# Optimization experiments

Hardware: AMD Instinct MI355X
Metric: run time of the kernel (lower is better)

Reference implementation:

```python
import jax, jax.numpy as jnp
import numpy as np

T, B, H, V, L = 512, 8, 256, 32000, 3
THRESH = 1.0

# Heaviside spike with ATan surrogate gradient (snntorch default, alpha=2)
@jax.custom_vjp
def spike(u):
    return (u > 0).astype(u.dtype)

def _spike_fwd(u):
    return (u > 0).astype(u.dtype), u

def _spike_bwd(u, g):
    return (g / (1.0 + (jnp.pi * u) ** 2),)

spike.defvjp(_spike_fwd, _spike_bwd)


def leaky_scan(cur, beta):
    """mem[t] = beta * mem[t-1] + cur[t]; cur: (T,B,H), beta: (H,). No reset -> associative."""
    def step(mem, c):
        mem = beta * mem + c
        return mem, mem
    _, mems = jax.lax.scan(step, jnp.zeros(cur.shape[1:], cur.dtype), cur)
    return mems  # (T,B,H)


def setup_inputs() -> dict:
    key = jax.random.key(0)
    ks = jax.random.split(key, 10)
    s = 1.0 / np.sqrt(H)
    return {
        "tokens": jax.random.randint(ks[0], (T, B), 0, V),
        "token_emb": jax.random.normal(ks[1], (V, H), dtype=jnp.float32) * 0.02,
        "pos_emb": jax.random.normal(ks[2], (T, H), dtype=jnp.float32) * 0.02,
        "Wq": jax.random.normal(ks[3], (L, H, H), dtype=jnp.float32) * s,
        "bq": jnp.zeros((L, H), dtype=jnp.float32),
        "beta": jax.random.uniform(ks[4], (L, H), minval=0.5, maxval=0.95),
        "Wfc": jax.random.normal(ks[5], (L, H, H), dtype=jnp.float32) * s,
        "bfc": jnp.zeros((L, H), dtype=jnp.float32),
        "Wout": jax.random.normal(ks[6], (H, V), dtype=jnp.float32) * s,
        "bout": jnp.zeros((V,), dtype=jnp.float32),
    }


def reference(tokens, token_emb, pos_emb, Wq, bq, beta, Wfc, bfc, Wout, bout):
    # embed: (T,B,H) + broadcast positional (T,1,H)
    h = token_emb[tokens] + pos_emb[:, None, :]
    for l in range(L):  # small fixed layer count
        cur = jnp.einsum('tbh,hd->tbd', h, Wq[l]) + bq[l]   # q-projection
        mem = leaky_scan(cur, beta[l])                       # leaky integrate, no reset
        spk = spike(mem - THRESH)                            # heaviside spikes
        h = jax.nn.relu(jnp.einsum('tbh,hd->tbd', spk, Wfc[l]) + bfc[l])
    logits = jnp.einsum('tbh,hv->tbv', h, Wout) + bout       # (T,B,V)
    return logits
```

## Files before the change

kernel.cpp:

```cpp
#include <hip/hip_runtime.h>
#include <hip/hip_bf16.h>
#include <cstddef>

constexpr int T_ = 512;
constexpr int B_ = 8;
constexpr int H_ = 256;
constexpr int V_ = 32000;
constexpr int L_ = 3;
constexpr int M_ = T_ * B_;

typedef __attribute__((ext_vector_type(8))) short short8;
typedef __attribute__((ext_vector_type(4))) float floatx4;

__device__ __forceinline__ unsigned short f2bf(float f) {
    unsigned u = __float_as_uint(f);
    u += 0x7fffu + ((u >> 16) & 1u);
    return (unsigned short)(u >> 16);
}

__device__ __forceinline__ void gl_lds16(const void* g, void* l) {
    __builtin_amdgcn_global_load_lds((__attribute__((address_space(1))) void*)g,
                                     (__attribute__((address_space(3))) void*)l,
                                     16, 0, 0);
}

__global__ __launch_bounds__(256) void embed_kernel(
    const int* __restrict__ tokens, const float* __restrict__ temb,
    const float* __restrict__ pemb, unsigned short* __restrict__ hb)
{
    const int idx = blockIdx.x * 256 + threadIdx.x;
    const int h4 = idx & (H_ / 4 - 1);
    const int tb = idx >> 6;
    const int b  = tb & (B_ - 1);
    const int t  = tb >> 3;
    const int tok = tokens[t * B_ + b];
    const float4 e = *(const float4*)&temb[(size_t)tok * H_ + h4 * 4];
    const float4 p = *(const float4*)&pemb[(size_t)t * H_ + h4 * 4];
    ushort4 r;
    r.x = f2bf(e.x + p.x); r.y = f2bf(e.y + p.y);
    r.z = f2bf(e.z + p.z); r.w = f2bf(e.w + p.w);
    *(ushort4*)&hb[(size_t)idx * 4] = r;
}

__global__ __launch_bounds__(256) void scan_spike_lds(
    const float* __restrict__ cur, const float* __restrict__ beta_l,
    unsigned short* __restrict__ spk)
{
    __shared__ float buf[2][32][256];
    const int b = blockIdx.x;
    const int tid = threadIdx.x;
    const float bt = beta_l[tid];
    const float* base = cur + (size_t)b * H_;
    unsigned short* qb = spk + (size_t)b * H_ + tid;
    constexpr int CH = 32;
    constexpr int NC = T_ / CH;
    constexpr size_t TS = (size_t)B_ * H_;

    float4 regs[8];
    #pragma unroll
    for (int i = 0; i < 8; ++i) {
        const int fi = tid + 256 * i, r = fi >> 6, x = fi & 63;
        regs[i] = *(const float4*)&base[(size_t)r * TS + x * 4];
    }
    #pragma unroll
    for (int i = 0; i < 8; ++i) {
        const int fi = tid + 256 * i, r = fi >> 6, x = fi & 63;
        *(float4*)&buf[0][r][x * 4] = regs[i];
    }

    float mem = 0.0f;
    for (int c = 0; c < NC; ++c) {
        __syncthreads();
        if (c + 1 < NC) {
            #pragma unroll
            for (int i = 0; i < 8; ++i) {
                const int fi = tid + 256 * i, r = fi >> 6, x = fi & 63;
                regs[i] = *(const float4*)&base[(size_t)((c + 1) * CH + r) * TS + x * 4];
            }
        }
        const int p = c & 1;
        #pragma unroll
        for (int tt = 0; tt < CH; ++tt) {
            mem = fmaf(bt, mem, buf[p][tt][tid]);
            qb[(size_t)(c * CH + tt) * TS] = (mem > 1.0f) ? (unsigned short)0x3F80u
                                                          : (unsigned short)0u;
        }
        if (c + 1 < NC) {
            #pragma unroll
            for (int i = 0; i < 8; ++i) {
                const int fi = tid + 256 * i, r = fi >> 6, x = fi & 63;
                *(float4*)&buf[(c + 1) & 1][r][x * 4] = regs[i];
            }
        }
    }
}

__global__ __launch_bounds__(256) void transpose_small_kernel(
    const float* __restrict__ Wq, const float* __restrict__ Wfc,
    unsigned short* __restrict__ WT)
{
    __shared__ float t[64][65];
    const int z = blockIdx.z;
    const float* src = (z < 3) ? Wq + (size_t)z * H_ * H_
                               : Wfc + (size_t)(z - 3) * H_ * H_;
    unsigned short* dst = WT + (size_t)z * H_ * H_;
    const int n0 = blockIdx.x * 64, k0 = blockIdx.y * 64;
    const int x = threadIdx.x & 63, y = threadIdx.x >> 6;
    #pragma unroll
    for (int i = 0; i < 16; ++i)
        t[y + 4 * i][x] = src[(size_t)(k0 + y + 4 * i) * H_ + n0 + x];
    __syncthreads();
    #pragma unroll
    for (int i = 0; i < 16; ++i)
        dst[(size_t)(n0 + y + 4 * i) * H_ + k0 + x] = f2bf(t[x][y + 4 * i]);
}

__global__ __launch_bounds__(256) void transpose_wout_kernel(
    const float* __restrict__ W, unsigned short* __restrict__ Wt)
{
    __shared__ float t[64][65];
    const int n0 = blockIdx.x * 64;
    const int k0 = blockIdx.y * 64;
    const int x = threadIdx.x & 63, y = threadIdx.x >> 6;
    #pragma unroll
    for (int i = 0; i < 16; ++i)
        t[y + 4 * i][x] = W[(size_t)(k0 + y + 4 * i) * V_ + n0 + x];
    __syncthreads();
    #pragma unroll
    for (int i = 0; i < 16; ++i)
        Wt[(size_t)(n0 + y + 4 * i) * H_ + k0 + x] = f2bf(t[x][y + 4 * i]);
}


__global__ __launch_bounds__(256) void gemm_mfma_out(
    const unsigned short* __restrict__ A,
    const unsigned short* __restrict__ Bt,
    const float* __restrict__ bias,
    float* __restrict__ C)
{
    constexpr int K = H_, N = V_;
    __shared__ __align__(16) short lA[1024][8];
    __shared__ __align__(16) short lB[1024][8];

    const int tid = threadIdx.x;
    const int lane = tid & 63, wave = tid >> 6;
    const int wm = wave >> 1, wn = wave & 1;
    const int l15 = lane & 15, quad = lane >> 4;
    const int m0 = blockIdx.x * 128;
    const int n0 = blockIdx.y * 128;

    floatx4 acc[4][4] = {};

    for (int k0 = 0; k0 < K; k0 += 64) {
        #pragma unroll
        for (int j = 0; j < 4; ++j) {
            const int base = (wave * 4 + j) * 64;
            const int s = base + lane;
            const int row = s >> 3;
            const int oct = (s & 7) ^ (row & 7);
            gl_lds16(A  + (size_t)(m0 + row) * K + k0 + oct * 8, &lA[base][0]);
            gl_lds16(Bt + (size_t)(n0 + row) * K + k0 + oct * 8, &lB[base][0]);
        }
        __syncthreads();

        #pragma unroll
        for (int t = 0; t < 2; ++t) {
            short8 af[4], bf[4];
            #pragma unroll
            for (int f = 0; f < 4; ++f) {
                const int ra = wm * 64 + f * 16 + l15;
                const int rb = wn * 64 + f * 16 + l15;
                af[f] = *(const short8*)&lA[ra * 8 + ((4 * t + quad) ^ (ra & 7))][0];
                bf[f] = *(const short8*)&lB[rb * 8 + ((4 * t + quad) ^ (rb & 7))][0];
            }
            #pragma unroll
            for (int i = 0; i < 4; ++i)
                #pragma unroll
                for (int j2 = 0; j2 < 4; ++j2)
                    acc[i][j2] = __builtin_amdgcn_mfma_f32_16x16x32_bf16(
                        af[i], bf[j2], acc[i][j2], 0, 0, 0);
        }
        __syncthreads();
    }

    #pragma unroll
    for (int j2 = 0; j2 < 4; ++j2) {
        const int col = n0 + wn * 64 + j2 * 16 + l15;
        const float bv = bias[col];
        #pragma unroll
        for (int i = 0; i < 4; ++i) {
            const int rbase = m0 + wm * 64 + i * 16 + quad * 4;
            #pragma unroll
            for (int r = 0; r < 4; ++r)
                C[(size_t)(rbase + r) * N + col] = acc[i][j2][r] + bv;
        }
    }
}

template <int RELU, int OUT_BF16>
__global__ __launch_bounds__(256) void gemm_mfma_layer(
    const unsigned short* __restrict__ A,
    const unsigned short* __restrict__ Bt,
    const float* __restrict__ bias,
    float* __restrict__ Cf, unsigned short* __restrict__ Cb)
{
    constexpr int K = H_, N = H_;
    __shared__ __align__(16) short lA[1024][8];
    __shared__ __align__(16) short lB[512][8];

    const int tid = threadIdx.x;
    const int lane = tid & 63, wave = tid >> 6;
    const int wm = wave >> 1, wn = wave & 1;
    const int l15 = lane & 15, quad = lane >> 4;
    const int m0 = blockIdx.x * 128;
    const int n0 = blockIdx.y * 64;

    floatx4 acc[4][2] = {};

    for (int k0 = 0; k0 < K; k0 += 64) {
        #pragma unroll
        for (int j = 0; j < 4; ++j) {
            const int base = (wave * 4 + j) * 64;
            const int s = base + lane;
            const int row = s >> 3;
            const int oct = (s & 7) ^ (row & 7);
            gl_lds16(A + (size_t)(m0 + row) * K + k0 + oct * 8, &lA[base][0]);
        }
        #pragma unroll
        for (int j = 0; j < 2; ++j) {
            const int base = (wave * 2 + j) * 64;
            const int s = base + lane;
            const int row = s >> 3;
            const int oct = (s & 7) ^ (row & 7);
            gl_lds16(Bt + (size_t)(n0 + row) * K + k0 + oct * 8, &lB[base][0]);
        }
        __syncthreads();

        #pragma unroll
        for (int t = 0; t < 2; ++t) {
            short8 af[4], bf[2];
            #pragma unroll
            for (int f = 0; f < 4; ++f) {
                const int ra = wm * 64 + f * 16 + l15;
                af[f] = *(const short8*)&lA[ra * 8 + ((4 * t + quad) ^ (ra & 7))][0];
            }
            #pragma unroll
            for (int f = 0; f < 2; ++f) {
                const int rb = wn * 32 + f * 16 + l15;
                bf[f] = *(const short8*)&lB[rb * 8 + ((4 * t + quad) ^ (rb & 7))][0];
            }
            #pragma unroll
            for (int i = 0; i < 4; ++i)
                #pragma unroll
                for (int j2 = 0; j2 < 2; ++j2)
                    acc[i][j2] = __builtin_amdgcn_mfma_f32_16x16x32_bf16(
                        af[i], bf[j2], acc[i][j2], 0, 0, 0);
        }
        __syncthreads();
    }

    #pragma unroll
    for (int j2 = 0; j2 < 2; ++j2) {
        const int col = n0 + wn * 32 + j2 * 16 + l15;
        const float bv = bias[col];
        #pragma unroll
        for (int i = 0; i < 4; ++i) {
            const int rbase = m0 + wm * 64 + i * 16 + quad * 4;
            #pragma unroll
            for (int r = 0; r < 4; ++r) {
                float v = acc[i][j2][r] + bv;
                if (RELU) v = fmaxf(v, 0.0f);
                if (OUT_BF16)
                    Cb[(size_t)(rbase + r) * N + col] = f2bf(v);
                else
                    Cf[(size_t)(rbase + r) * N + col] = v;
            }
        }
    }
}

extern "C" void kernel_launch(void* const* d_in, const int* in_sizes, int n_in,
                              void* d_out, int out_size, void* d_ws, size_t ws_size,
                              hipStream_t stream)
{
    const int*   tokens = (const int*)  d_in[0];
    const float* temb   = (const float*)d_in[1];
    const float* pemb   = (const float*)d_in[2];
    const float* Wq     = (const float*)d_in[3];
    const float* bq     = (const float*)d_in[4];
    const float* beta   = (const float*)d_in[5];
    const float* Wfc    = (const float*)d_in[6];
    const float* bfc    = (const float*)d_in[7];
    const float* Wout   = (const float*)d_in[8];
    const float* bout   = (const float*)d_in[9];
    float* out = (float*)d_out;

    unsigned short* h_bf  = (unsigned short*)d_ws;
    unsigned short* spk   = h_bf + (size_t)M_ * H_;
    unsigned short* WT    = spk + (size_t)M_ * H_;
    unsigned short* WoutT = WT + (size_t)2 * L_ * H_ * H_;
    float*          cur   = (float*)(WoutT + (size_t)V_ * H_);

    transpose_small_kernel<<<dim3(4, 4, 6), 256, 0, stream>>>(Wq, Wfc, WT);
    transpose_wout_kernel<<<dim3(V_ / 64, H_ / 64), 256, 0, stream>>>(Wout, WoutT);

    embed_kernel<<<(M_ * H_ / 4) / 256, 256, 0, stream>>>(tokens, temb, pemb, h_bf);

    for (int l = 0; l < L_; ++l) {
        const unsigned short* WqT  = WT + (size_t)l * H_ * H_;
        const unsigned short* WfcT = WT + (size_t)(L_ + l) * H_ * H_;
        gemm_mfma_layer<0, 0><<<dim3(M_ / 128, H_ / 64), 256, 0, stream>>>(
            h_bf, WqT, bq + (size_t)l * H_, cur, nullptr);
        scan_spike_lds<<<B_, 256, 0, stream>>>(cur, beta + (size_t)l * H_, spk);
        gemm_mfma_layer<1, 1><<<dim3(M_ / 128, H_ / 64), 256, 0, stream>>>(
            spk, WfcT, bfc + (size_t)l * H_, nullptr, h_bf);
    }

    gemm_mfma_out<<<dim3(M_ / 128, V_ / 128), 256, 0, stream>>>(
        h_bf, WoutT, bout, out);
}
```

Measured before the change: 751.8 us.

## Parallelize leaky scan over time chunks with two-pass chunked scan

Replaces the single-pass scan, which used only B=8 blocks and walked all 512 timesteps sequentially, with a two-kernel chunked scan. The first kernel computes local prefix sums within 32-step chunks across 16x8 blocks. The second propagates carries from earlier chunk ends using beta^32 and applies them with beta powers before thresholding. This raises parallelism from 8 to 128 blocks, at the cost of an extra fp32 intermediate round trip, one more launch, and slightly different floating-point rounding near the threshold.

```diff
diff --git a/kernel.cpp b/kernel.cpp
--- a/kernel.cpp
+++ b/kernel.cpp
@@ -42,56 +42,50 @@
     *(ushort4*)&hb[(size_t)idx * 4] = r;
 }
 
-__global__ __launch_bounds__(256) void scan_spike_lds(
+constexpr int CH_ = 32;
+constexpr int NT_ = T_ / CH_;
+constexpr int TS_ = B_ * H_;
+
+__global__ __launch_bounds__(256) void scan_local_kernel(
     const float* __restrict__ cur, const float* __restrict__ beta_l,
+    float* __restrict__ mloc)
+{
+    const int c = blockIdx.x, b = blockIdx.y, h = threadIdx.x;
+    const float bt = beta_l[h];
+    const size_t off = ((size_t)(c * CH_) * B_ + b) * H_ + h;
+    const float* p = cur + off;
+    float* q = mloc + off;
+    float mem = 0.0f;
+    #pragma unroll
+    for (int tt = 0; tt < CH_; ++tt) {
+        mem = fmaf(bt, mem, p[(size_t)tt * TS_]);
+        q[(size_t)tt * TS_] = mem;
+    }
+}
+
+__global__ __launch_bounds__(256) void scan_apply_kernel(
+    const float* __restrict__ mloc, const float* __restrict__ beta_l,
     unsigned short* __restrict__ spk)
 {
-    __shared__ float buf[2][32][256];
-    const int b = blockIdx.x;
-    const int tid = threadIdx.x;
-    const float bt = beta_l[tid];
-    const float* base = cur + (size_t)b * H_;
-    unsigned short* qb = spk + (size_t)b * H_ + tid;
-    constexpr int CH = 32;
-    constexpr int NC = T_ / CH;
-    constexpr size_t TS = (size_t)B_ * H_;
-
-    float4 regs[8];
-    #pragma unroll
-    for (int i = 0; i < 8; ++i) {
-        const int fi = tid + 256 * i, r = fi >> 6, x = fi & 63;
-        regs[i] = *(const float4*)&base[(size_t)r * TS + x * 4];
-    }
-    #pragma unroll
-    for (int i = 0; i < 8; ++i) {
-        const int fi = tid + 256 * i, r = fi >> 6, x = fi & 63;
-        *(float4*)&buf[0][r][x * 4] = regs[i];
-    }
-
-    float mem = 0.0f;
-    for (int c = 0; c < NC; ++c) {
-        __syncthreads();
-        if (c + 1 < NC) {
-            #pragma unroll
-            for (int i = 0; i < 8; ++i) {
-                const int fi = tid + 256 * i, r = fi >> 6, x = fi & 63;
-                regs[i] = *(const float4*)&base[(size_t)((c + 1) * CH + r) * TS + x * 4];
-            }
-        }
-        const int p = c & 1;
-        #pragma unroll
-        for (int tt = 0; tt < CH; ++tt) {
-            mem = fmaf(bt, mem, buf[p][tt][tid]);
-            qb[(size_t)(c * CH + tt) * TS] = (mem > 1.0f) ? (unsigned short)0x3F80u
-                                                          : (unsigned short)0u;
-        }
-        if (c + 1 < NC) {
-            #pragma unroll
-            for (int i = 0; i < 8; ++i) {
-                const int fi = tid + 256 * i, r = fi >> 6, x = fi & 63;
-                *(float4*)&buf[(c + 1) & 1][r][x * 4] = regs[i];
-            }
-        }
+    const int c = blockIdx.x, b = blockIdx.y, h = threadIdx.x;
+    const float bt = beta_l[h];
+    float b32 = bt;
+    #pragma unroll
+    for (int i = 0; i < 5; ++i) b32 *= b32;
+    float carry = 0.0f;
+    for (int j = 0; j < c; ++j)
+        carry = fmaf(b32, carry,
+                     mloc[((size_t)(j * CH_ + CH_ - 1) * B_ + b) * H_ + h]);
+    const size_t off = ((size_t)(c * CH_) * B_ + b) * H_ + h;
+    const float* p = mloc + off;
+    unsigned short* q = spk + off;
+    float pw = bt;
+    #pragma unroll
+    for (int tt = 0; tt < CH_; ++tt) {
+        const float mem = fmaf(pw, carry, p[(size_t)tt * TS_]);
+        pw *= bt;
+        q[(size_t)tt * TS_] = (mem > 1.0f) ? (unsigned short)0x3F80u
+                                           : (unsigned short)0u;
     }
 }
 
@@ -300,6 +294,7 @@
     unsigned short* WT    = spk + (size_t)M_ * H_;
     unsigned short* WoutT = WT + (size_t)2 * L_ * H_ * H_;
     float*          cur   = (float*)(WoutT + (size_t)V_ * H_);
+    float*          mloc  = cur + (size_t)M_ * H_;
 
     transpose_small_kernel<<<dim3(4, 4, 6), 256, 0, stream>>>(Wq, Wfc, WT);
     transpose_wout_kernel<<<dim3(V_ / 64, H_ / 64), 256, 0, stream>>>(Wout, WoutT);
@@ -311,7 +306,10 @@
         const unsigned short* WfcT = WT + (size_t)(L_ + l) * H_ * H_;
         gemm_mfma_layer<0, 0><<<dim3(M_ / 128, H_ / 64), 256, 0, stream>>>(
             h_bf, WqT, bq + (size_t)l * H_, cur, nullptr);
-        scan_spike_lds<<<B_, 256, 0, stream>>>(cur, beta + (size_t)l * H_, spk);
+        scan_local_kernel<<<dim3(NT_, B_), 256, 0, stream>>>(
+            cur, beta + (size_t)l * H_, mloc);
+        scan_apply_kernel<<<dim3(NT_, B_), 256, 0, stream>>>(
+            mloc, beta + (size_t)l * H_, spk);
         gemm_mfma_layer<1, 1><<<dim3(M_ / 128, H_ / 64), 256, 0, stream>>>(
             spk, WfcT, bfc + (size_t)l * H_, nullptr, h_bf);
     }
```

New measurement: 738.2 us. Within noise of the previous version (-1.8%).
